# Kernel tuning notes

Hardware: AMD Instinct MI355X
Metric: run time of the kernel (lower is better)

## Reference

```python
import jax, jax.numpy as jnp
import numpy as np

N_NODES = 50000
N_EDGES = 800000
D_FEAT = 96


def setup_inputs() -> dict:
    key = jax.random.key(0)
    k1, k2, k3, k4 = jax.random.split(key, 4)
    rows = jax.random.randint(k1, (N_EDGES,), 0, N_NODES, dtype=jnp.int64)
    cols = jax.random.randint(k2, (N_EDGES,), 0, N_NODES, dtype=jnp.int64)
    # nonnegative edge weights, as in a normalized adjacency
    vals = jax.random.uniform(k3, (N_EDGES,), dtype=jnp.float32)
    embeds = jax.random.normal(k4, (N_NODES, D_FEAT), dtype=jnp.float32)
    return {"rows": rows, "cols": cols, "vals": vals, "embeds": embeds}


def reference(rows, cols, vals, embeds):
    # out = adj @ embeds, adj given in COO form (rows, cols, vals)
    # gather source-node embeddings, scale by edge weight, scatter-add to dst
    msgs = vals[:, None] * embeds[cols]          # [E, d]
    out = jax.ops.segment_sum(msgs, rows, num_segments=embeds.shape[0])  # [N, d]
    return out
```

## Files before the change

### kernel.cpp

```cpp
#include <hip/hip_runtime.h>


#define DFEAT    96
#define BINSHIFT 5
#define BINROWS  32
#define MAXBIN   2048
#define EPB      4096
#define SCT      1024
#define CAP      1024

__device__ inline unsigned bf16_rne(float x) {
    unsigned u = __float_as_uint(x);
    return (u + 0x7FFFu + ((u >> 16) & 1u)) >> 16;
}
__device__ inline float bf16_to_f32(unsigned short u) {
    return __uint_as_float((unsigned)u << 16);
}

__global__ void hist_bin_compress_kernel(const int* __restrict__ rows,
                                         int* __restrict__ matrix, int E, int B, int nbin,
                                         const float* __restrict__ embeds,
                                         unsigned short* __restrict__ ebf, int nOct) {
    __shared__ int cnt[MAXBIN];
    int b = blockIdx.x;
    if (b < B) {
        for (int k = threadIdx.x; k < nbin; k += blockDim.x) cnt[k] = 0;
        __syncthreads();
        int base = b * EPB;
        int lim  = min(base + EPB, E);
        for (int i = base + threadIdx.x; i < lim; i += blockDim.x)
            atomicAdd(&cnt[rows[i] >> BINSHIFT], 1);
        __syncthreads();
        for (int k = threadIdx.x; k < nbin; k += blockDim.x)
            matrix[(size_t)k * B + b] = cnt[k];
    } else {
        int j = (b - B) * blockDim.x + threadIdx.x;
        if (j < nOct) {
            const float4* src = reinterpret_cast<const float4*>(embeds) + (size_t)j * 2;
            float4 f0 = src[0];
            float4 f1 = src[1];
            uint4 o;
            o.x = bf16_rne(f0.x) | (bf16_rne(f0.y) << 16);
            o.y = bf16_rne(f0.z) | (bf16_rne(f0.w) << 16);
            o.z = bf16_rne(f1.x) | (bf16_rne(f1.y) << 16);
            o.w = bf16_rne(f1.z) | (bf16_rne(f1.w) << 16);
            reinterpret_cast<uint4*>(ebf)[j] = o;
        }
    }
}

__global__ void scan1024_kernel(int* __restrict__ data, int* __restrict__ bsums, int n) {
    __shared__ int s[SCT];
    int t = threadIdx.x;
    int i = blockIdx.x * SCT + t;
    int v = (i < n) ? data[i] : 0;
    s[t] = v;
    __syncthreads();
    for (int off = 1; off < SCT; off <<= 1) {
        int u = (t >= off) ? s[t - off] : 0;
        __syncthreads();
        s[t] += u;
        __syncthreads();
    }
    if (i < n) data[i] = s[t] - v;
    if (t == SCT - 1) bsums[blockIdx.x] = s[t];
}

__global__ void scan_sums1024_kernel(int* __restrict__ bsums, int nb) {
    __shared__ int s[SCT];
    int t = threadIdx.x;
    int v = (t < nb) ? bsums[t] : 0;
    s[t] = v;
    __syncthreads();
    for (int off = 1; off < SCT; off <<= 1) {
        int u = (t >= off) ? s[t - off] : 0;
        __syncthreads();
        s[t] += u;
        __syncthreads();
    }
    if (t < nb) bsums[t] = s[t] - v;
}

__device__ inline int scanned_at(const int* __restrict__ matrixScan,
                                 const int* __restrict__ bsums, long long flatIdx) {
    return matrixScan[flatIdx] + bsums[flatIdx >> 10];
}

__global__ void scatter_bin_kernel(const int* __restrict__ rows, const int* __restrict__ cols,
                                   const float* __restrict__ vals,
                                   const int* __restrict__ matrixScan,
                                   const int* __restrict__ bsums,
                                   int2* __restrict__ bucket, int E, int B, int nbin) {
    __shared__ int cur[MAXBIN];
    int b = blockIdx.x;
    for (int k = threadIdx.x; k < nbin; k += blockDim.x)
        cur[k] = scanned_at(matrixScan, bsums, (long long)k * B + b);
    __syncthreads();
    int base = b * EPB;
    int lim  = min(base + EPB, E);
    for (int i = base + threadIdx.x; i < lim; i += blockDim.x) {
        int r = rows[i];
        int bin = r >> BINSHIFT;
        int pos = atomicAdd(&cur[bin], 1);
        bucket[pos] = make_int2(((r & (BINROWS - 1)) << 16) | cols[i],
                                __float_as_int(vals[i]));
    }
}

__global__ void sortaccum_kernel(const int2* __restrict__ bucket,
                                 const int* __restrict__ matrixScan,
                                 const int* __restrict__ bsums,
                                 const unsigned short* __restrict__ ebf,
                                 float* __restrict__ out, int E, int B, int nbin, int N) {
    __shared__ int2 sorted[CAP];
    __shared__ int cnt[BINROWS];
    __shared__ int segs[BINROWS];
    __shared__ int cur[BINROWS];
    __shared__ int s32[BINROWS];

    int bin = blockIdx.x;
    int t = threadIdx.x;
    int hw = t >> 5;
    int lane = t & 31;

    int start = scanned_at(matrixScan, bsums, (long long)bin * B);
    int end   = (bin + 1 < nbin) ? scanned_at(matrixScan, bsums, (long long)(bin + 1) * B) : E;

    float acc[4][3];
    #pragma unroll
    for (int rr = 0; rr < 4; ++rr) { acc[rr][0] = 0.f; acc[rr][1] = 0.f; acc[rr][2] = 0.f; }

    for (int cs = start; cs < end; cs += CAP) {
        int m = min(CAP, end - cs);

        if (t < BINROWS) cnt[t] = 0;
        __syncthreads();

        int2 ee[4];
        #pragma unroll
        for (int k = 0; k < 4; ++k) {
            int j = t + k * 256;
            if (j < m) {
                ee[k] = bucket[cs + j];
                atomicAdd(&cnt[ee[k].x >> 16], 1);
            }
        }
        __syncthreads();

        if (t < BINROWS) s32[t] = cnt[t];
        __syncthreads();
        for (int off = 1; off < BINROWS; off <<= 1) {
            int u = (t < BINROWS && t >= off) ? s32[t - off] : 0;
            __syncthreads();
            if (t < BINROWS) s32[t] += u;
            __syncthreads();
        }
        if (t < BINROWS) {
            int ex = s32[t] - cnt[t];
            segs[t] = ex;
            cur[t]  = ex;
        }
        __syncthreads();

        #pragma unroll
        for (int k = 0; k < 4; ++k) {
            int j = t + k * 256;
            if (j < m) {
                int pos = atomicAdd(&cur[ee[k].x >> 16], 1);
                sorted[pos] = make_int2((ee[k].x & 0xFFFF) * DFEAT, ee[k].y);
            }
        }
        __syncthreads();

        #pragma unroll
        for (int rr = 0; rr < 4; ++rr) {
            int r = hw * 4 + rr;
            int j  = segs[r];
            int je = segs[r] + cnt[r];
            for (; j + 4 <= je; j += 4) {
                int2 p0 = sorted[j];
                int2 p1 = sorted[j + 1];
                int2 p2 = sorted[j + 2];
                int2 p3 = sorted[j + 3];
                float v0 = __int_as_float(p0.y), v1 = __int_as_float(p1.y);
                float v2 = __int_as_float(p2.y), v3 = __int_as_float(p3.y);
                float x0 = bf16_to_f32(ebf[p0.x + lane]);
                float y0 = bf16_to_f32(ebf[p0.x + lane + 32]);
                float z0 = bf16_to_f32(ebf[p0.x + lane + 64]);
                float x1 = bf16_to_f32(ebf[p1.x + lane]);
                float y1 = bf16_to_f32(ebf[p1.x + lane + 32]);
                float z1 = bf16_to_f32(ebf[p1.x + lane + 64]);
                float x2 = bf16_to_f32(ebf[p2.x + lane]);
                float y2 = bf16_to_f32(ebf[p2.x + lane + 32]);
                float z2 = bf16_to_f32(ebf[p2.x + lane + 64]);
                float x3 = bf16_to_f32(ebf[p3.x + lane]);
                float y3 = bf16_to_f32(ebf[p3.x + lane + 32]);
                float z3 = bf16_to_f32(ebf[p3.x + lane + 64]);
                acc[rr][0] += v0 * x0 + v1 * x1;
                acc[rr][1] += v0 * y0 + v1 * y1;
                acc[rr][2] += v0 * z0 + v1 * z1;
                acc[rr][0] += v2 * x2 + v3 * x3;
                acc[rr][1] += v2 * y2 + v3 * y3;
                acc[rr][2] += v2 * z2 + v3 * z3;
            }
            for (; j < je; ++j) {
                int2 p = sorted[j];
                float v = __int_as_float(p.y);
                acc[rr][0] += v * bf16_to_f32(ebf[p.x + lane]);
                acc[rr][1] += v * bf16_to_f32(ebf[p.x + lane + 32]);
                acc[rr][2] += v * bf16_to_f32(ebf[p.x + lane + 64]);
            }
        }
        __syncthreads();
    }

    int row0 = bin << BINSHIFT;
    #pragma unroll
    for (int rr = 0; rr < 4; ++rr) {
        int row = row0 + hw * 4 + rr;
        if (row < N) {
            float* o = out + (size_t)row * DFEAT;
            o[lane]      = acc[rr][0];
            o[lane + 32] = acc[rr][1];
            o[lane + 64] = acc[rr][2];
        }
    }
}

__global__ void gcn_scatter_atomic_kernel(const int* __restrict__ rows, const int* __restrict__ cols,
                                          const float* __restrict__ vals, const float* __restrict__ embeds,
                                          float* __restrict__ out, int n_edges) {
    long long i = (long long)blockIdx.x * blockDim.x + threadIdx.x;
    long long total = (long long)n_edges * (DFEAT / 4);
    if (i >= total) return;
    int e = (int)(i / (DFEAT / 4));
    int q = (int)(i - (long long)e * (DFEAT / 4));
    int r = rows[e], c = cols[e];
    float v = vals[e];
    const float4* emb4 = reinterpret_cast<const float4*>(embeds + (long long)c * DFEAT);
    float4 x = emb4[q];
    float* o = out + (long long)r * DFEAT + q * 4;
    atomicAdd(o + 0, v * x.x);
    atomicAdd(o + 1, v * x.y);
    atomicAdd(o + 2, v * x.z);
    atomicAdd(o + 3, v * x.w);
}

extern "C" void kernel_launch(void* const* d_in, const int* in_sizes, int n_in,
                              void* d_out, int out_size, void* d_ws, size_t ws_size,
                              hipStream_t stream) {
    const int*   rows   = (const int*)d_in[0];
    const int*   cols   = (const int*)d_in[1];
    const float* vals   = (const float*)d_in[2];
    const float* embeds = (const float*)d_in[3];
    float*       out    = (float*)d_out;

    int E = in_sizes[0];
    int N = in_sizes[3] / DFEAT;

    int nbin  = (N + BINROWS - 1) >> BINSHIFT;
    int B     = (E + EPB - 1) / EPB;
    long long flatN = (long long)nbin * B;
    int SB    = (int)((flatN + SCT - 1) / SCT);

    size_t off_matrix = 0;
    size_t off_bsums  = (off_matrix + (size_t)flatN * 4 + 15) & ~(size_t)15;
    size_t off_bucket = (off_bsums + (size_t)SB * 4 + 15) & ~(size_t)15;
    size_t off_ebf    = (off_bucket + (size_t)E * 8 + 63) & ~(size_t)63;
    size_t need       = off_ebf + (size_t)N * DFEAT * 2;

    bool ok = (N <= 65536) && (nbin <= MAXBIN) && (SB <= SCT) &&
              ((in_sizes[3] & 7) == 0) && (ws_size >= need);

    if (ok) {
        int*  matrix = (int*)((char*)d_ws + off_matrix);
        int*  bsums  = (int*)((char*)d_ws + off_bsums);
        int2* bucket = (int2*)((char*)d_ws + off_bucket);
        unsigned short* ebf = (unsigned short*)((char*)d_ws + off_ebf);

        int nOct = in_sizes[3] / 8;
        int cb   = (nOct + 255) / 256;

        hist_bin_compress_kernel<<<B + cb, 256, 0, stream>>>(
            rows, matrix, E, B, nbin, embeds, ebf, nOct);

        scan1024_kernel<<<SB, SCT, 0, stream>>>(matrix, bsums, (int)flatN);
        scan_sums1024_kernel<<<1, SCT, 0, stream>>>(bsums, SB);

        scatter_bin_kernel<<<B, 256, 0, stream>>>(rows, cols, vals, matrix, bsums,
                                                  bucket, E, B, nbin);

        sortaccum_kernel<<<nbin, 256, 0, stream>>>(bucket, matrix, bsums, ebf, out,
                                                   E, B, nbin, N);
    } else {
        hipMemsetAsync(d_out, 0, (size_t)out_size * sizeof(float), stream);
        long long total = (long long)E * (DFEAT / 4);
        int block = 256;
        long long grid = (total + block - 1) / block;
        gcn_scatter_atomic_kernel<<<(int)grid, block, 0, stream>>>(rows, cols, vals, embeds, out, E);
    }
}
```

Before: 65.20 us.

## Shrink edges per binning block and scan four counters per thread

Edges per histogram/scatter block drop from 4096 to 1024, giving roughly four times as many blocks in the binning kernels so more compute units are busy. The count matrix grows by the same factor, so the prefix scan now handles 4096 elements per block with vectorized int4 loads and stores, and the block-sum index shift changes to match. The trade-off is a larger count matrix to write, scan and read back, plus more per-block work initializing the bin counters relative to the edges each block handles.

```diff
diff --git a/kernel.cpp b/kernel.cpp
--- a/kernel.cpp
+++ b/kernel.cpp
@@ -5,8 +5,8 @@
 #define BINSHIFT 5
 #define BINROWS  32
 #define MAXBIN   2048
-#define EPB      4096
-#define SCT      1024
+#define EPB      1024
+#define SCHUNK   4096
 #define CAP      1024
 
 __device__ inline unsigned bf16_rne(float x) {
@@ -49,30 +49,49 @@
     }
 }
 
-__global__ void scan1024_kernel(int* __restrict__ data, int* __restrict__ bsums, int n) {
-    __shared__ int s[SCT];
+__global__ void scan4096_kernel(int* __restrict__ data, int* __restrict__ bsums, int n) {
+    __shared__ int s[1024];
     int t = threadIdx.x;
-    int i = blockIdx.x * SCT + t;
-    int v = (i < n) ? data[i] : 0;
-    s[t] = v;
+    long long base = (long long)blockIdx.x * SCHUNK + (long long)t * 4;
+    int v0 = 0, v1 = 0, v2 = 0, v3 = 0;
+    if (base + 3 < n) {
+        int4 q = *reinterpret_cast<const int4*>(data + base);
+        v0 = q.x; v1 = q.y; v2 = q.z; v3 = q.w;
+    } else {
+        if (base     < n) v0 = data[base];
+        if (base + 1 < n) v1 = data[base + 1];
+        if (base + 2 < n) v2 = data[base + 2];
+        if (base + 3 < n) v3 = data[base + 3];
+    }
+    int sum = v0 + v1 + v2 + v3;
+    s[t] = sum;
     __syncthreads();
-    for (int off = 1; off < SCT; off <<= 1) {
+    for (int off = 1; off < 1024; off <<= 1) {
         int u = (t >= off) ? s[t - off] : 0;
         __syncthreads();
         s[t] += u;
         __syncthreads();
     }
-    if (i < n) data[i] = s[t] - v;
-    if (t == SCT - 1) bsums[blockIdx.x] = s[t];
+    int excl = s[t] - sum;
+    int p0 = excl, p1 = excl + v0, p2 = p1 + v1, p3 = p2 + v2;
+    if (base + 3 < n) {
+        *reinterpret_cast<int4*>(data + base) = make_int4(p0, p1, p2, p3);
+    } else {
+        if (base     < n) data[base]     = p0;
+        if (base + 1 < n) data[base + 1] = p1;
+        if (base + 2 < n) data[base + 2] = p2;
+        if (base + 3 < n) data[base + 3] = p3;
+    }
+    if (t == 1023) bsums[blockIdx.x] = s[1023];
 }
 
 __global__ void scan_sums1024_kernel(int* __restrict__ bsums, int nb) {
-    __shared__ int s[SCT];
+    __shared__ int s[1024];
     int t = threadIdx.x;
     int v = (t < nb) ? bsums[t] : 0;
     s[t] = v;
     __syncthreads();
-    for (int off = 1; off < SCT; off <<= 1) {
+    for (int off = 1; off < 1024; off <<= 1) {
         int u = (t >= off) ? s[t - off] : 0;
         __syncthreads();
         s[t] += u;
@@ -83,7 +102,7 @@
 
 __device__ inline int scanned_at(const int* __restrict__ matrixScan,
                                  const int* __restrict__ bsums, long long flatIdx) {
-    return matrixScan[flatIdx] + bsums[flatIdx >> 10];
+    return matrixScan[flatIdx] + bsums[flatIdx >> 12];
 }
 
 __global__ void scatter_bin_kernel(const int* __restrict__ rows, const int* __restrict__ cols,
@@ -261,7 +280,7 @@
     int nbin  = (N + BINROWS - 1) >> BINSHIFT;
     int B     = (E + EPB - 1) / EPB;
     long long flatN = (long long)nbin * B;
-    int SB    = (int)((flatN + SCT - 1) / SCT);
+    int SB    = (int)((flatN + SCHUNK - 1) / SCHUNK);
 
     size_t off_matrix = 0;
     size_t off_bsums  = (off_matrix + (size_t)flatN * 4 + 15) & ~(size_t)15;
@@ -269,7 +288,7 @@
     size_t off_ebf    = (off_bucket + (size_t)E * 8 + 63) & ~(size_t)63;
     size_t need       = off_ebf + (size_t)N * DFEAT * 2;
 
-    bool ok = (N <= 65536) && (nbin <= MAXBIN) && (SB <= SCT) &&
+    bool ok = (N <= 65536) && (nbin <= MAXBIN) && (SB <= 1024) &&
               ((in_sizes[3] & 7) == 0) && (ws_size >= need);
 
     if (ok) {
@@ -284,8 +303,8 @@
         hist_bin_compress_kernel<<<B + cb, 256, 0, stream>>>(
             rows, matrix, E, B, nbin, embeds, ebf, nOct);
 
-        scan1024_kernel<<<SB, SCT, 0, stream>>>(matrix, bsums, (int)flatN);
-        scan_sums1024_kernel<<<1, SCT, 0, stream>>>(bsums, SB);
+        scan4096_kernel<<<SB, 1024, 0, stream>>>(matrix, bsums, (int)flatN);
+        scan_sums1024_kernel<<<1, 1024, 0, stream>>>(bsums, SB);
 
         scatter_bin_kernel<<<B, 256, 0, stream>>>(rows, cols, vals, matrix, bsums,
                                                   bucket, E, B, nbin);
```

After: 71.90 us. +10.3%, slower.
